# Optimization experiments

Hardware: AMD Instinct MI355X
Metric: run time of the kernel (lower is better)

## Reference

```python
import jax, jax.numpy as jnp
import numpy as np

GRID_SIZE = 64
SPLINE_ORDER = 3
NUM_BASIS = GRID_SIZE + SPLINE_ORDER - 1  # 66
GRID_MIN, GRID_MAX = -1.0, 1.0
EPS = 1e-7
B, IN_F, OUT_F = 4096, 256, 256


def setup_inputs() -> dict:
    key = jax.random.key(0)
    k1, k2, k3, k4 = jax.random.split(key, 4)
    x = jax.random.normal(k1, (B, IN_F), dtype=jnp.float32)
    base_weight = jax.random.normal(k2, (IN_F, OUT_F), dtype=jnp.float32) * (1.0 / np.sqrt(IN_F))
    scale = 1.0 / np.sqrt(NUM_BASIS)
    spline_weight = jax.random.uniform(k3, (IN_F, OUT_F, NUM_BASIS), dtype=jnp.float32, minval=-scale, maxval=scale)
    spline_scaler = jax.random.uniform(k4, (IN_F, OUT_F), dtype=jnp.float32)
    return {"x": x, "base_weight": base_weight, "spline_weight": spline_weight, "spline_scaler": spline_scaler}


def _spline_basis(x):
    # normalize to [0,1], map onto grid coordinate
    x_c = jnp.clip(x, GRID_MIN, GRID_MAX)
    x_norm = (x_c - GRID_MIN) / (GRID_MAX - GRID_MIN + EPS)
    x_scaled = x_norm * (GRID_SIZE - 1)
    grid_idx = jnp.clip(jnp.floor(x_scaled), 0.0, GRID_SIZE - SPLINE_ORDER)
    local_x = x_scaled - grid_idx                                  # [B, in]
    centers = jnp.linspace(0.0, 1.0, NUM_BASIS, dtype=jnp.float32)  # [nb]
    sigma = 1.0 / NUM_BASIS
    bv = jnp.exp(-jnp.square(local_x[..., None] - centers) / (2.0 * sigma * sigma))  # [B, in, nb]
    # (safe_mode clip is skipped at inference: training falsy)
    bv = bv / (jnp.sum(bv, axis=-1, keepdims=True) + EPS)
    return bv


def reference(x, base_weight, spline_weight, spline_scaler):
    base_out = x @ base_weight                                     # [B, out]
    basis = _spline_basis(x)                                       # [B, in, nb]
    # sum over basis then over in_features: same math as the expanded
    # elementwise-product/sum chain in the original call()
    spline_out = jnp.einsum('bik,iok->bo', basis, spline_weight)   # [B, out]
    scaling = jnp.mean(jnp.maximum(spline_scaler, EPS), axis=0)    # [out]
    return base_out + spline_out * scaling
```

## Files before the change

kernel.cpp:

```cpp
#include <hip/hip_runtime.h>
#include <stdint.h>


#define IN_F 256
#define OUT_F 256
#define NB 66
#define KP 80
#define APAD 88
#define KSPLIT 8
#define SLABS 32
#define BM 64
#define NTHREADS 512
#define GRID_MAIN 512

typedef __attribute__((ext_vector_type(8))) short bf16x8;
typedef __attribute__((ext_vector_type(16))) float f32x16;

__device__ __forceinline__ unsigned int f2bf(float f) {
  unsigned int u = __float_as_uint(f);
  u += 0x7FFFu + ((u >> 16) & 1u);
  return u >> 16;
}

__global__ void kan_scale8(const float* __restrict__ sca, float* __restrict__ wsp) {
  const int o = threadIdx.x, b = blockIdx.x;
  float s = 0.0f;
  #pragma unroll
  for (int j = 0; j < 32; j++) {
    const int i = b * 32 + j;
    s += fmaxf(sca[(size_t)i * OUT_F + o], 1e-7f);
  }
  wsp[b * OUT_F + o] = s;
}

__global__ void kan_pack(const float* __restrict__ sw, const float* __restrict__ bw,
                         const float* __restrict__ wsp, unsigned short* __restrict__ wp2) {
  const int i = blockIdx.x, o = threadIdx.x;
  float sc = 0.0f;
  #pragma unroll
  for (int b = 0; b < 8; b++) sc += wsp[b * OUT_F + o];
  sc *= (1.0f / 256.0f);
  const float2* src = (const float2*)(sw + ((size_t)i * OUT_F + o) * NB);
  float v[80];
  #pragma unroll
  for (int j = 0; j < 33; j++) {
    float2 t2 = src[j];
    v[2 * j] = t2.x * sc;
    v[2 * j + 1] = t2.y * sc;
  }
  v[66] = bw[(size_t)i * OUT_F + o];
  #pragma unroll
  for (int k = 67; k < 80; k++) v[k] = 0.0f;
  uint4* dst = (uint4*)wp2;
  #pragma unroll
  for (int g = 0; g < 10; g++) {
    uint4 u;
    unsigned int* up = (unsigned int*)&u;
    #pragma unroll
    for (int h = 0; h < 4; h++)
      up[h] = f2bf(v[g * 8 + 2 * h]) | (f2bf(v[g * 8 + 2 * h + 1]) << 16);
    dst[((size_t)i * 10 + g) * OUT_F + o] = u;
  }
}

__global__ __launch_bounds__(NTHREADS, 4) void kan_main(
    const float* __restrict__ x, const unsigned short* __restrict__ wp2,
    float* __restrict__ dst, int atomic_mode) {
  __shared__ unsigned short A[2][BM * APAD];

  const int t = threadIdx.x;
  const int lane = t & 63;
  const int w = t >> 6;
  const int ml = lane & 31;
  const int half = lane >> 5;
  const int mblk = (int)blockIdx.x >> 3;
  const int kidx = (int)blockIdx.x & 7;
  const int b0 = mblk * BM;
  const int ibase = kidx * SLABS;

  const int rb = t >> 3;
  const int q = t & 7;
  const int ks = (q + (q > 0) + (q > 4)) * 8;
  const int len = ((q & 3) == 0) ? 16 : 8;
  const int nchunk = len >> 3;

  const float* xrow = x + (size_t)(b0 + rb) * IN_F;
  const int boff = (w * 32 + ml) * 8;

  bf16x8 breg[2][5];
  f32x16 acc[2] = {f32x16{}, f32x16{}};

#define LOADB(P, ISLAB)                                                        \
  {                                                                            \
    const unsigned short* bp =                                                 \
        wp2 + (size_t)(ISLAB) * (OUT_F * KP) + half * 2048 + boff;             \
    _Pragma("unroll") for (int kk = 0; kk < 5; kk++) {                         \
      breg[P][kk] = *(const bf16x8*)(bp + kk * 4096);                          \
    }                                                                          \
  }

#define BASIS(BUFSEL, XVAL)                                                    \
  {                                                                            \
    const float xr_ = (XVAL);                                                  \
    const float xc_ = fminf(fmaxf(xr_, -1.0f), 1.0f);                          \
    const float xs_ = (xc_ + 1.0f) * (63.0f / (2.0f + 1e-7f));                 \
    const float tl_ = xs_ - fminf(floorf(xs_), 61.0f);                         \
    float e_[16];                                                              \
    float s_ = 0.0f;                                                           \
    _Pragma("unroll") for (int j = 0; j < 16; j++) {                           \
      const int k = ks + j;                                                    \
      const float d_ = tl_ - (float)k * (1.0f / 65.0f);                        \
      float ee = __expf(-2178.0f * d_ * d_);                                   \
      ee = (j < len && k < 66) ? ee : 0.0f;                                    \
      e_[j] = ee;                                                              \
      s_ += ee;                                                                \
    }                                                                          \
    s_ += __shfl_xor(s_, 1);                                                   \
    s_ += __shfl_xor(s_, 2);                                                   \
    s_ += __shfl_xor(s_, 4);                                                   \
    const float r_ = __fdividef(1.0f, s_ + 1e-7f);                             \
    unsigned short* Ar = &A[BUFSEL][rb * APAD + ks];                           \
    _Pragma("unroll") for (int c = 0; c < 2; c++) {                            \
      if (c < nchunk) {                                                        \
        uint4 u;                                                               \
        unsigned int* up = (unsigned int*)&u;                                  \
        _Pragma("unroll") for (int h = 0; h < 4; h++) {                        \
          const int k0 = ks + c * 8 + h * 2;                                   \
          float f0 = e_[c * 8 + h * 2] * r_;                                   \
          float f1 = e_[c * 8 + h * 2 + 1] * r_;                               \
          f0 = (k0 == 66) ? xr_ : f0;                                          \
          f1 = (k0 + 1 == 66) ? xr_ : f1;                                      \
          up[h] = f2bf(f0) | (f2bf(f1) << 16);                                 \
        }                                                                      \
        *(uint4*)(Ar + c * 8) = u;                                             \
      }                                                                        \
    }                                                                          \
  }

#define MFMA_SLAB(CUR, P)                                                      \
  {                                                                            \
    const unsigned short* Ac = &A[CUR][0];                                     \
    _Pragma("unroll") for (int kk = 0; kk < 5; kk++) {                         \
      const int ko = kk * 16 + half * 8;                                       \
      bf16x8 a0 = *(const bf16x8*)(Ac + ml * APAD + ko);                       \
      bf16x8 a1 = *(const bf16x8*)(Ac + (32 + ml) * APAD + ko);                \
      acc[0] = __builtin_amdgcn_mfma_f32_32x32x16_bf16(a0, breg[P][kk], acc[0], 0, 0, 0); \
      acc[1] = __builtin_amdgcn_mfma_f32_32x32x16_bf16(a1, breg[P][kk], acc[1], 0, 0, 0); \
    }                                                                          \
  }

  BASIS(0, xrow[ibase]);
  LOADB(0, ibase);
  float xn = xrow[ibase + 1];
  __syncthreads();

#define STEP(II, P)                                                            \
  {                                                                            \
    if ((II) + 1 < SLABS) LOADB(1 - (P), ibase + (II) + 1);                    \
    MFMA_SLAB((II) & 1, P);                                                    \
    const float xc2 = xn;                                                      \
    if ((II) + 2 < SLABS) xn = xrow[ibase + (II) + 2];                         \
    if ((II) + 1 < SLABS) BASIS(((II) + 1) & 1, xc2);                          \
    __syncthreads();                                                           \
  }

  for (int ii = 0; ii < SLABS; ii += 2) {
    STEP(ii, 0);
    STEP(ii + 1, 1);
  }

  const int colb = w * 32 + ml;
  if (atomic_mode) {
    #pragma unroll
    for (int mb = 0; mb < 2; mb++) {
      #pragma unroll
      for (int r = 0; r < 16; r++) {
        const int row = b0 + mb * 32 + (r & 3) + 8 * (r >> 2) + 4 * half;
        atomicAdd(&dst[(size_t)row * OUT_F + colb], acc[mb][r]);
      }
    }
  } else {
    float* pd = dst + (size_t)kidx * ((size_t)4096 * OUT_F);
    #pragma unroll
    for (int mb = 0; mb < 2; mb++) {
      #pragma unroll
      for (int r = 0; r < 16; r++) {
        const int row = b0 + mb * 32 + (r & 3) + 8 * (r >> 2) + 4 * half;
        pd[(size_t)row * OUT_F + colb] = acc[mb][r];
      }
    }
  }
}

__global__ void kan_reduce(const float* __restrict__ part, float* __restrict__ out) {
  const size_t j = ((size_t)blockIdx.x * 256 + threadIdx.x) * 4;
  float4 a = *(const float4*)(part + j);
  #pragma unroll
  for (int s = 1; s < 8; s++) {
    float4 b = *(const float4*)(part + (size_t)s * 1048576 + j);
    a.x += b.x; a.y += b.y; a.z += b.z; a.w += b.w;
  }
  *(float4*)(out + j) = a;
}

__global__ void kan_naive(const float* __restrict__ x, const float* __restrict__ bw,
                          const float* __restrict__ sw, const float* __restrict__ sca,
                          float* __restrict__ out) {
  const int o = threadIdx.x;
  const int b = blockIdx.x;
  float accb = 0.0f, accs = 0.0f, scl = 0.0f;
  for (int i = 0; i < IN_F; i++) {
    const float xraw = x[(size_t)b * IN_F + i];
    accb += xraw * bw[(size_t)i * OUT_F + o];
    scl += fmaxf(sca[(size_t)i * OUT_F + o], 1e-7f);
    const float xc = fminf(fmaxf(xraw, -1.0f), 1.0f);
    const float xs = (xc + 1.0f) * (63.0f / (2.0f + 1e-7f));
    const float tl = xs - fminf(floorf(xs), 61.0f);
    const int kc = (int)(tl * 65.0f + 0.5f);
    const int k0 = max(0, min(kc - 8, 50));
    float e[16]; float s = 0.0f;
    #pragma unroll
    for (int j = 0; j < 16; j++) {
      float d = tl - (float)(k0 + j) * (1.0f / 65.0f);
      e[j] = __expf(-2178.0f * d * d);
      s += e[j];
    }
    const float r = __fdividef(1.0f, s + 1e-7f);
    const float* wrow = sw + ((size_t)i * OUT_F + o) * NB + k0;
    float dot = 0.0f;
    #pragma unroll
    for (int j = 0; j < 16; j++) dot += e[j] * wrow[j];
    accs += dot * r;
  }
  out[(size_t)b * OUT_F + o] = accb + accs * (scl * (1.0f / 256.0f));
}

extern "C" void kernel_launch(void* const* d_in, const int* in_sizes, int n_in,
                              void* d_out, int out_size, void* d_ws, size_t ws_size,
                              hipStream_t stream) {
  const float* x   = (const float*)d_in[0];
  const float* bw  = (const float*)d_in[1];
  const float* sw  = (const float*)d_in[2];
  const float* sca = (const float*)d_in[3];
  float* out = (float*)d_out;

  const size_t WP2_BYTES  = (size_t)IN_F * OUT_F * KP * 2;
  const size_t WP_OFF     = 8192;
  const size_t PART_OFF   = WP_OFF + WP2_BYTES;
  const size_t PART_BYTES = (size_t)KSPLIT * 4096 * OUT_F * 4;

  if (ws_size >= PART_OFF + PART_BYTES) {
    float* wsp = (float*)d_ws;
    unsigned short* wp2 = (unsigned short*)((char*)d_ws + WP_OFF);
    float* part = (float*)((char*)d_ws + PART_OFF);
    kan_scale8<<<8, 256, 0, stream>>>(sca, wsp);
    kan_pack<<<256, 256, 0, stream>>>(sw, bw, wsp, wp2);
    kan_main<<<GRID_MAIN, NTHREADS, 0, stream>>>(x, wp2, part, 0);
    kan_reduce<<<1024, 256, 0, stream>>>(part, out);
  } else if (ws_size >= PART_OFF) {
    float* wsp = (float*)d_ws;
    unsigned short* wp2 = (unsigned short*)((char*)d_ws + WP_OFF);
    hipMemsetAsync(d_out, 0, (size_t)out_size * sizeof(float), stream);
    kan_scale8<<<8, 256, 0, stream>>>(sca, wsp);
    kan_pack<<<256, 256, 0, stream>>>(sw, bw, wsp, wp2);
    kan_main<<<GRID_MAIN, NTHREADS, 0, stream>>>(x, wp2, out, 1);
  } else {
    kan_naive<<<4096, 256, 0, stream>>>(x, bw, sw, sca, out);
  }
}
```

Before: 157.6 us.

## Sparse basis window, packed bf16 cvt, contiguous weight layout, fused scale reduction

The basis computation now evaluates the exponential only for a 24-entry window around the nearest centre and writes zeros elsewhere, cutting per-element exp work. The weight pack uses the v_cvt_pk_bf16_f32 instruction and a layout where each lane's five B fragments are contiguous, loaded through an advancing pointer with single buffering. The separate scaler-reduction kernel is folded into kan_pack, with each thread summing all 256 rows, which removes a launch but repeats that reduction in every block. Truncating the Gaussian to the window drops tails that are negligible in bf16, so results may differ slightly from the full sum.

Result: slower. 185.1 us (+17.4%).

```diff
diff --git a/kernel.cpp b/kernel.cpp
--- a/kernel.cpp
+++ b/kernel.cpp
@@ -16,29 +16,19 @@
 typedef __attribute__((ext_vector_type(8))) short bf16x8;
 typedef __attribute__((ext_vector_type(16))) float f32x16;
 
-__device__ __forceinline__ unsigned int f2bf(float f) {
-  unsigned int u = __float_as_uint(f);
-  u += 0x7FFFu + ((u >> 16) & 1u);
-  return u >> 16;
-}
-
-__global__ void kan_scale8(const float* __restrict__ sca, float* __restrict__ wsp) {
-  const int o = threadIdx.x, b = blockIdx.x;
-  float s = 0.0f;
-  #pragma unroll
-  for (int j = 0; j < 32; j++) {
-    const int i = b * 32 + j;
-    s += fmaxf(sca[(size_t)i * OUT_F + o], 1e-7f);
-  }
-  wsp[b * OUT_F + o] = s;
+__device__ __forceinline__ unsigned int cvtpk(float lo, float hi) {
+  unsigned int r;
+  asm("v_cvt_pk_bf16_f32 %0, %1, %2" : "=v"(r) : "v"(lo), "v"(hi));
+  return r;
 }
 
 __global__ void kan_pack(const float* __restrict__ sw, const float* __restrict__ bw,
-                         const float* __restrict__ wsp, unsigned short* __restrict__ wp2) {
+                         const float* __restrict__ sca, unsigned short* __restrict__ wp2) {
   const int i = blockIdx.x, o = threadIdx.x;
   float sc = 0.0f;
-  #pragma unroll
-  for (int b = 0; b < 8; b++) sc += wsp[b * OUT_F + o];
+  #pragma unroll 8
+  for (int ii = 0; ii < IN_F; ii++)
+    sc += fmaxf(sca[(size_t)ii * OUT_F + o], 1e-7f);
   sc *= (1.0f / 256.0f);
   const float2* src = (const float2*)(sw + ((size_t)i * OUT_F + o) * NB);
   float v[80];
@@ -53,13 +43,16 @@
   for (int k = 67; k < 80; k++) v[k] = 0.0f;
   uint4* dst = (uint4*)wp2;
   #pragma unroll
-  for (int g = 0; g < 10; g++) {
-    uint4 u;
-    unsigned int* up = (unsigned int*)&u;
-    #pragma unroll
-    for (int h = 0; h < 4; h++)
-      up[h] = f2bf(v[g * 8 + 2 * h]) | (f2bf(v[g * 8 + 2 * h + 1]) << 16);
-    dst[((size_t)i * 10 + g) * OUT_F + o] = u;
+  for (int half = 0; half < 2; half++) {
+    #pragma unroll
+    for (int kk = 0; kk < 5; kk++) {
+      const float* p = v + kk * 16 + half * 8;
+      uint4 u;
+      unsigned int* up = (unsigned int*)&u;
+      #pragma unroll
+      for (int h = 0; h < 4; h++) up[h] = cvtpk(p[2 * h], p[2 * h + 1]);
+      dst[(((size_t)i * 2 + half) * 256 + o) * 5 + kk] = u;
+    }
   }
 }
 
@@ -80,23 +73,19 @@
 
   const int rb = t >> 3;
   const int q = t & 7;
-  const int ks = (q + (q > 0) + (q > 4)) * 8;
-  const int len = ((q & 3) == 0) ? 16 : 8;
-  const int nchunk = len >> 3;
 
   const float* xrow = x + (size_t)(b0 + rb) * IN_F;
-  const int boff = (w * 32 + ml) * 8;
-
-  bf16x8 breg[2][5];
+  const unsigned short* bptr =
+      wp2 + (((size_t)ibase * 2 + half) * 256 + (w * 32 + ml)) * 40;
+
+  bf16x8 breg[5];
   f32x16 acc[2] = {f32x16{}, f32x16{}};
 
-#define LOADB(P, ISLAB)                                                        \
+#define LOADB_ADV()                                                            \
   {                                                                            \
-    const unsigned short* bp =                                                 \
-        wp2 + (size_t)(ISLAB) * (OUT_F * KP) + half * 2048 + boff;             \
-    _Pragma("unroll") for (int kk = 0; kk < 5; kk++) {                         \
-      breg[P][kk] = *(const bf16x8*)(bp + kk * 4096);                          \
-    }                                                                          \
+    _Pragma("unroll") for (int kk = 0; kk < 5; kk++)                           \
+      breg[kk] = *(const bf16x8*)(bptr + kk * 8);                              \
+    bptr += 20480;                                                             \
   }
 
 #define BASIS(BUFSEL, XVAL)                                                    \
@@ -105,68 +94,77 @@
     const float xc_ = fminf(fmaxf(xr_, -1.0f), 1.0f);                          \
     const float xs_ = (xc_ + 1.0f) * (63.0f / (2.0f + 1e-7f));                 \
     const float tl_ = xs_ - fminf(floorf(xs_), 61.0f);                         \
-    float e_[16];                                                              \
+    const int ikc_ = min((int)(tl_ * 65.0f + 0.5f), 65);                       \
+    const int g0_ = max((ikc_ - 8) >> 3, 0);                                   \
+    unsigned short* Arow_ = &A[BUFSEL][rb * APAD];                             \
+    const int kbase_ = (g0_ + q) * 8;                                          \
+    float e_[8];                                                               \
     float s_ = 0.0f;                                                           \
-    _Pragma("unroll") for (int j = 0; j < 16; j++) {                           \
-      const int k = ks + j;                                                    \
-      const float d_ = tl_ - (float)k * (1.0f / 65.0f);                        \
-      float ee = __expf(-2178.0f * d_ * d_);                                   \
-      ee = (j < len && k < 66) ? ee : 0.0f;                                    \
-      e_[j] = ee;                                                              \
-      s_ += ee;                                                                \
+    if (q < 3) {                                                               \
+      const float tb_ = tl_ - (float)kbase_ * (1.0f / 65.0f);                  \
+      _Pragma("unroll") for (int j = 0; j < 8; j++) {                          \
+        const float d_ = tb_ - (float)j * (1.0f / 65.0f);                      \
+        float ee = __builtin_amdgcn_exp2f(-3142.1892f * d_ * d_);              \
+        ee = (kbase_ + j < 66) ? ee : 0.0f;                                    \
+        e_[j] = ee;                                                            \
+        s_ += ee;                                                              \
+      }                                                                        \
     }                                                                          \
     s_ += __shfl_xor(s_, 1);                                                   \
     s_ += __shfl_xor(s_, 2);                                                   \
     s_ += __shfl_xor(s_, 4);                                                   \
     const float r_ = __fdividef(1.0f, s_ + 1e-7f);                             \
-    unsigned short* Ar = &A[BUFSEL][rb * APAD + ks];                           \
-    _Pragma("unroll") for (int c = 0; c < 2; c++) {                            \
-      if (c < nchunk) {                                                        \
-        uint4 u;                                                               \
-        unsigned int* up = (unsigned int*)&u;                                  \
-        _Pragma("unroll") for (int h = 0; h < 4; h++) {                        \
-          const int k0 = ks + c * 8 + h * 2;                                   \
-          float f0 = e_[c * 8 + h * 2] * r_;                                   \
-          float f1 = e_[c * 8 + h * 2 + 1] * r_;                               \
-          f0 = (k0 == 66) ? xr_ : f0;                                          \
-          f1 = (k0 + 1 == 66) ? xr_ : f1;                                      \
-          up[h] = f2bf(f0) | (f2bf(f1) << 16);                                 \
-        }                                                                      \
-        *(uint4*)(Ar + c * 8) = u;                                             \
+    if (q < 3) {                                                               \
+      uint4 u_;                                                                \
+      unsigned int* up_ = (unsigned int*)&u_;                                  \
+      _Pragma("unroll") for (int h = 0; h < 4; h++) {                          \
+        float f0 = e_[2 * h] * r_;                                             \
+        const float f1 = e_[2 * h + 1] * r_;                                   \
+        f0 = (kbase_ + 2 * h == 66) ? xr_ : f0;                                \
+        up_[h] = cvtpk(f0, f1);                                                \
+      }                                                                        \
+      *(uint4*)(Arow_ + kbase_) = u_;                                          \
+    } else {                                                                   \
+      const unsigned int bu_ = cvtpk(xr_, 0.0f);                               \
+      const int zq_ = q - 3;                                                   \
+      const int zg_ = (zq_ < g0_) ? zq_ : zq_ + 3;                             \
+      uint4 z_ = {0u, 0u, 0u, 0u};                                             \
+      uint4 b_ = {0u, bu_, 0u, 0u};         \
+      *(uint4*)(Arow_ + zg_ * 8) = (zg_ == 8) ? b_ : z_;                       \
+      if (zq_ < 2) {                                                           \
+        const int zg2_ = (zq_ + 5 < g0_) ? zq_ + 5 : zq_ + 8;                  \
+        *(uint4*)(Arow_ + zg2_ * 8) = (zg2_ == 8) ? b_ : z_;                   \
       }                                                                        \
     }                                                                          \
   }
 
-#define MFMA_SLAB(CUR, P)                                                      \
+#define MFMA_SLAB(CUR)                                                         \
   {                                                                            \
     const unsigned short* Ac = &A[CUR][0];                                     \
     _Pragma("unroll") for (int kk = 0; kk < 5; kk++) {                         \
       const int ko = kk * 16 + half * 8;                                       \
       bf16x8 a0 = *(const bf16x8*)(Ac + ml * APAD + ko);                       \
       bf16x8 a1 = *(const bf16x8*)(Ac + (32 + ml) * APAD + ko);                \
-      acc[0] = __builtin_amdgcn_mfma_f32_32x32x16_bf16(a0, breg[P][kk], acc[0], 0, 0, 0); \
-      acc[1] = __builtin_amdgcn_mfma_f32_32x32x16_bf16(a1, breg[P][kk], acc[1], 0, 0, 0); \
+      acc[0] = __builtin_amdgcn_mfma_f32_32x32x16_bf16(a0, breg[kk], acc[0], 0, 0, 0); \
+      acc[1] = __builtin_amdgcn_mfma_f32_32x32x16_bf16(a1, breg[kk], acc[1], 0, 0, 0); \
     }                                                                          \
   }
 
   BASIS(0, xrow[ibase]);
-  LOADB(0, ibase);
+  LOADB_ADV();
   float xn = xrow[ibase + 1];
   __syncthreads();
 
-#define STEP(II, P)                                                            \
-  {                                                                            \
-    if ((II) + 1 < SLABS) LOADB(1 - (P), ibase + (II) + 1);                    \
-    MFMA_SLAB((II) & 1, P);                                                    \
-    const float xc2 = xn;                                                      \
-    if ((II) + 2 < SLABS) xn = xrow[ibase + (II) + 2];                         \
-    if ((II) + 1 < SLABS) BASIS(((II) + 1) & 1, xc2);                          \
-    __syncthreads();                                                           \
-  }
-
-  for (int ii = 0; ii < SLABS; ii += 2) {
-    STEP(ii, 0);
-    STEP(ii + 1, 1);
+  #pragma unroll 2
+  for (int ii = 0; ii < SLABS; ii++) {
+    MFMA_SLAB(ii & 1);
+    if (ii + 1 < SLABS) {
+      LOADB_ADV();
+      const float xc2 = xn;
+      if (ii + 2 < SLABS) xn = xrow[ibase + ii + 2];
+      BASIS((ii + 1) & 1, xc2);
+    }
+    __syncthreads();
   }
 
   const int colb = w * 32 + ml;
@@ -245,24 +243,18 @@
   float* out = (float*)d_out;
 
   const size_t WP2_BYTES  = (size_t)IN_F * OUT_F * KP * 2;
-  const size_t WP_OFF     = 8192;
-  const size_t PART_OFF   = WP_OFF + WP2_BYTES;
   const size_t PART_BYTES = (size_t)KSPLIT * 4096 * OUT_F * 4;
 
-  if (ws_size >= PART_OFF + PART_BYTES) {
-    float* wsp = (float*)d_ws;
-    unsigned short* wp2 = (unsigned short*)((char*)d_ws + WP_OFF);
-    float* part = (float*)((char*)d_ws + PART_OFF);
-    kan_scale8<<<8, 256, 0, stream>>>(sca, wsp);
-    kan_pack<<<256, 256, 0, stream>>>(sw, bw, wsp, wp2);
+  if (ws_size >= WP2_BYTES + PART_BYTES) {
+    unsigned short* wp2 = (unsigned short*)d_ws;
+    float* part = (float*)((char*)d_ws + WP2_BYTES);
+    kan_pack<<<256, 256, 0, stream>>>(sw, bw, sca, wp2);
     kan_main<<<GRID_MAIN, NTHREADS, 0, stream>>>(x, wp2, part, 0);
     kan_reduce<<<1024, 256, 0, stream>>>(part, out);
-  } else if (ws_size >= PART_OFF) {
-    float* wsp = (float*)d_ws;
-    unsigned short* wp2 = (unsigned short*)((char*)d_ws + WP_OFF);
-    hipMemsetAsync(d_out, 0, (size_t)out_size * sizeof(float), stream);
-    kan_scale8<<<8, 256, 0, stream>>>(sca, wsp);
-    kan_pack<<<256, 256, 0, stream>>>(sw, bw, wsp, wp2);
+  } else if (ws_size >= WP2_BYTES) {
+    unsigned short* wp2 = (unsigned short*)d_ws;
+    (void)hipMemsetAsync(d_out, 0, (size_t)out_size * sizeof(float), stream);
+    kan_pack<<<256, 256, 0, stream>>>(sw, bw, sca, wp2);
     kan_main<<<GRID_MAIN, NTHREADS, 0, stream>>>(x, wp2, out, 1);
   } else {
     kan_naive<<<4096, 256, 0, stream>>>(x, bw, sw, sca, out);
```
